# Kernel tuning notes

Measured on AMD Instinct MI355X. Metric: run time of the kernel, lower is better.

Reference implementation:

```python
import jax, jax.numpy as jnp
import numpy as np

# hypercfg constants (init_kwargs)
AUX = 0.05
L1W = 5.0
VPW = 1.0
VNW = 1.0


def _lsa_square(cost):
    """Jonker-Volgenant shortest-augmenting-path Hungarian on a square numpy
    cost matrix. Returns rows[j] = row assigned to column j. Runs on host,
    mirroring the original CPU scipy.optimize.linear_sum_assignment call."""
    n = cost.shape[0]
    INF = np.inf
    u = np.zeros(n + 1)
    v = np.zeros(n + 1)
    p = np.zeros(n + 1, dtype=np.int64)   # p[j] = row matched to column j (1-indexed)
    way = np.zeros(n + 1, dtype=np.int64)
    for i in range(1, n + 1):
        p[0] = i
        j0 = 0
        minv = np.full(n + 1, INF)
        used = np.zeros(n + 1, dtype=bool)
        while True:
            used[j0] = True
            i0 = p[j0]
            cur = cost[i0 - 1, :] - u[i0] - v[1:]
            free = ~used[1:]
            upd = free & (cur < minv[1:])
            minv1 = minv[1:]
            minv1[upd] = cur[upd]
            way1 = way[1:]
            way1[upd] = j0
            mfree = np.where(free, minv1, INF)
            j1 = int(np.argmin(mfree)) + 1
            delta = mfree[j1 - 1]
            used_idx = np.nonzero(used)[0]
            u[p[used_idx]] += delta
            v[used_idx] -= delta
            minv1[free] -= delta
            j0 = j1
            if p[j0] == 0:
                break
        while j0 != 0:
            j1 = way[j0]
            p[j0] = p[j1]
            j0 = j1
    return p[1:] - 1


def _match(cost_mk):
    """Rectangular assignment, cost [M, K] with K <= M: pad with a constant
    column block (dummy columns cost the same for any row, so the real K
    columns get the optimal assignment, matching scipy on rectangles)."""
    M, K = cost_mk.shape
    pad = np.zeros((M, M), dtype=np.float64)
    pad[:, :K] = cost_mk
    rows = _lsa_square(pad)
    return rows[:K]


def _cost(meta_points, meta_visibles, gtpoints, gtvisibles):
    # meta_points: [S,B,L,M,2]  gtpoints: [S,B,K,2]
    # meta_visibles: [S,B,M,1]  gtvisibles: [S,B,K,1]
    S, B, L, M, _ = meta_points.shape
    # pairwise L1 cost: [S,B,L,M,K]
    diff = jnp.abs(meta_points[:, :, :, :, None, :] - gtpoints[:, :, None, None, :, :]).sum(-1)
    # delta[l] = L - (l+1), per-layer slack (torch.linspace(1, L, L))
    delta = (L - jnp.arange(1, L + 1, dtype=meta_points.dtype)) * AUX
    cost_p_ml = jax.nn.relu(diff - delta[None, None, :, None, None])
    gtv = gtvisibles[:, :, :, 0][:, :, None, :]          # [S,B,1,K]
    cost_p = gtv * cost_p_ml.mean(2)                     # [S,B,M,K]
    cost_vp = -gtv * jnp.log(meta_visibles)              # [S,B,M,1] -> [S,B,M,K]
    cost_vn = -(1.0 - gtv) * jnp.log(1.0 - meta_visibles)
    cost = L1W * cost_p + VPW * cost_vp + VNW * cost_vn  # [S,B,M,K]
    return cost.mean(0)                                  # mean over shots -> [B,M,K]


def setup_inputs() -> dict:
    key = jax.random.key(0)
    ks = jax.random.split(key, 5)
    S, B, L, M, K = 6, 16, 8, 256, 128
    meta_points = jax.random.uniform(ks[0], (S, B, L, M, 2), dtype=jnp.float32)
    # keep probabilities strictly inside (0,1) so log() is finite
    meta_visibles = jax.random.uniform(ks[1], (S, B, M, 1), dtype=jnp.float32) * 0.9 + 0.05
    covisibles = jax.random.uniform(ks[2], (B, K), dtype=jnp.float32)
    gtpoints = jax.random.uniform(ks[3], (S, B, K, 2), dtype=jnp.float32)
    gtvisibles = (jax.random.uniform(ks[4], (S, B, K, 1)) > 0.5).astype(jnp.float32)
    return {
        "meta_points": meta_points,
        "meta_visibles": meta_visibles,
        "covisibles": covisibles,
        "gtpoints": gtpoints,
        "gtvisibles": gtvisibles,
    }


def reference(meta_points, meta_visibles, covisibles, gtpoints, gtvisibles):
    # covisibles only provides the batch size in the original module
    cost = np.asarray(jax.jit(_cost)(meta_points, meta_visibles, gtpoints, gtvisibles))
    bs = cost.shape[0]
    # per-batch Hungarian on host (sequential data-dependent algorithm);
    # result[b, k] = meta index matched to keypoint k (already kp-sorted,
    # matching the argsort-reorder in the torch code)
    out = np.stack([_match(cost[b]) for b in range(bs)])
    return jnp.asarray(out, dtype=jnp.int64)
```

## Files before the change

### kernel.cpp

```cpp
#include <hip/hip_runtime.h>
#include <math.h>


#define S_ 6
#define B_ 16
#define L_ 8
#define M_ 256
#define K_ 128

__global__ void cost_kernel(const float* __restrict__ mp,
                            const float* __restrict__ mv,
                            const float* __restrict__ gt,
                            const float* __restrict__ gv,
                            float* __restrict__ cost)
{
#pragma clang fp contract(off)
    const int b = blockIdx.x;
    const int m = blockIdx.y;
    const int k = threadIdx.x;

    float accS = 0.0f;
    for (int s = 0; s < S_; ++s) {
        const int sb = s * B_ + b;
        const float gx = gt[(sb * K_ + k) * 2 + 0];
        const float gy = gt[(sb * K_ + k) * 2 + 1];
        float accL = 0.0f;
#pragma unroll
        for (int l = 0; l < L_; ++l) {
            const int base = ((sb * L_ + l) * M_ + m) * 2;
            const float dx = fabsf(mp[base + 0] - gx);
            const float dy = fabsf(mp[base + 1] - gy);
            const float diff = dx + dy;
            const float dl = (float)(L_ - (l + 1)) * 0.05f;
            const float t = diff - dl;
            accL += fmaxf(t, 0.0f);
        }
        const float meanL = accL * 0.125f;
        const float mvv = mv[sb * M_ + m];
        const float gtv = gv[sb * K_ + k];
        const float lp = -logf(mvv);
        const float ln = -logf(1.0f - mvv);
        const float val = (gtv != 0.0f) ? (5.0f * meanL + lp) : ln;
        accS += val;
    }
    cost[(b * M_ + m) * K_ + k] = accS * (1.0f / 6.0f);
}

__device__ __forceinline__ double bits2d(int lo, int hi) {
    const unsigned long long u =
        ((unsigned long long)(unsigned)hi << 32) | (unsigned)lo;
    return __longlong_as_double((long long)u);
}
__device__ __forceinline__ void d2bits(double d, int& lo, int& hi) {
    const unsigned long long u = (unsigned long long)__double_as_longlong(d);
    lo = (int)(u & 0xffffffffull);
    hi = (int)(u >> 32);
}

__global__ __launch_bounds__(64, 1) void match_kernel(const float* __restrict__ cost,
                                                      int* __restrict__ out)
{
#pragma clang fp contract(off)
    const int b = blockIdx.x;
    const int lane = threadIdx.x;
    const float* C = cost + (size_t)b * M_ * K_;
    const double INF = __builtin_inf();
    const int BIG = 0x7fffffff;

    __shared__ float  C_lds[M_ * K_];
    __shared__ double u_lds[257];
    __shared__ int    p_lds[257];

    for (int t = lane; t < (M_ * K_) / 4; t += 64)
        ((float4*)C_lds)[t] = ((const float4*)C)[t];

    for (int t = lane; t < 257; t += 64) {
        u_lds[t] = 0.0;
        p_lds[t] = (t >= 129) ? (t - 128) : 0;
    }
    __syncthreads();

    double v0 = 0.0, v1 = 0.0, v2 = 0.0, v3 = 0.0;

    for (int i = 129; i <= 256; ++i) {
        int used = 0;
        const int pj0 = p_lds[2 * lane + 1];
        const int pj1 = p_lds[2 * lane + 2];
        const int pj2 = p_lds[2 * lane + 129];
        const int pj3 = p_lds[2 * lane + 130];
        double ur0 = u_lds[pj0], ur1 = u_lds[pj1];
        double ur2 = u_lds[pj2], ur3 = u_lds[pj3];
        const double up0 = ur0, up1 = ur1, up2 = ur2, up3 = ur3;

        float2 cc = *(const float2*)(C_lds + (i - 1) * K_ + 2 * lane);
        double u_i0 = 0.0;
        int j1 = 0;
        double usum = 0.0;

        for (;;) {
            double cd0 = ((double)cc.x - u_i0) - v0;
            double cd1 = ((double)cc.y - u_i0) - v1;
            double cd2 = (0.0 - u_i0) - v2;
            double cd3 = (0.0 - u_i0) - v3;
            if (used & 1) cd0 = INF;
            if (used & 2) cd1 = INF;
            if (used & 4) cd2 = INF;
            if (used & 8) cd3 = INF;

            const double m01 = fmin(cd0, cd1);
            const double m23 = fmin(cd2, cd3);
            double bv = fmin(m01, m23);

            int lo, hi; d2bits(bv, lo, hi);
#define MIN_STAGE(CTRL, RM)                                                      \
            {                                                                    \
                const int nlo = __builtin_amdgcn_update_dpp(lo, lo, CTRL, RM, 0xf, false); \
                const int nhi = __builtin_amdgcn_update_dpp(hi, hi, CTRL, RM, 0xf, false); \
                const double mv2 = fmin(bits2d(lo, hi), bits2d(nlo, nhi));       \
                d2bits(mv2, lo, hi);                                             \
            }
            MIN_STAGE(0x111, 0xf)
            MIN_STAGE(0x112, 0xf)
            MIN_STAGE(0x114, 0xf)
            MIN_STAGE(0x118, 0xf)
            MIN_STAGE(0x142, 0xa)
            MIN_STAGE(0x143, 0xc)
#undef MIN_STAGE
            const int mlo = __builtin_amdgcn_readlane(lo, 63);
            const int mhi = __builtin_amdgcn_readlane(hi, 63);
            const double delta = bits2d(mlo, mhi);

            int jr = BIG;
            if (cd1 == delta) jr = 2 * lane + 2;
            if (cd0 == delta) jr = 2 * lane + 1;
            int jd = BIG;
            if (cd3 == delta) jd = 2 * lane + 130;
            if (cd2 == delta) jd = 2 * lane + 129;
            const unsigned long long br = __ballot(jr != BIG);
            const unsigned long long bd = __ballot(jd != BIG);
            const unsigned long long bb = br ? br : bd;
            const int cand = (br != 0ull) ? jr : jd;
            j1 = __builtin_amdgcn_readlane(cand, (int)__builtin_ctzll(bb));

            int ol, sl;
            if (j1 >= 129) { ol = (j1 - 129) >> 1; sl = 2 + ((j1 - 129) & 1); }
            else           { ol = (j1 - 1) >> 1;   sl = (j1 - 1) & 1; }
            const int psel = (sl == 0) ? pj0 : (sl == 1) ? pj1 : (sl == 2) ? pj2 : pj3;
            const int i0n = (j1 >= 129) ? (j1 - 128)
                                        : __builtin_amdgcn_readlane(psel, ol);

            const int rown = (i0n > 0 ? i0n : 1) - 1;
            const float2 ccn = *(const float2*)(C_lds + rown * K_ + 2 * lane);

            usum += delta;
            if (used & 1) { ur0 += delta; v0 -= delta; }
            if (used & 2) { ur1 += delta; v1 -= delta; }
            if (used & 4) { ur2 += delta; v2 -= delta; }
            if (used & 8) { ur3 += delta; v3 -= delta; }

            const double usel = (sl == 0) ? up0 : (sl == 1) ? up1 : (sl == 2) ? up2 : up3;
            int ulo, uhi; d2bits(usel, ulo, uhi);
            const double u_n = bits2d(__builtin_amdgcn_readlane(ulo, ol),
                                      __builtin_amdgcn_readlane(uhi, ol));

            if (i0n == 0) break;

            if (lane == ol) used |= (1 << sl);
            u_i0 = u_n;
            cc = ccn;
        }

        __syncthreads();
        if (used & 1) u_lds[pj0] = ur0;
        if (used & 2) u_lds[pj1] = ur1;
        if (used & 4) u_lds[pj2] = ur2;
        if (used & 8) u_lds[pj3] = ur3;
        if (lane == 0) { p_lds[j1] = i; u_lds[i] = usum; }
        __syncthreads();
    }

    for (int j = lane; j < K_; j += 64)
        out[b * K_ + j] = p_lds[j + 1] - 1;
}

extern "C" void kernel_launch(void* const* d_in, const int* in_sizes, int n_in,
                              void* d_out, int out_size, void* d_ws, size_t ws_size,
                              hipStream_t stream) {
    const float* mp = (const float*)d_in[0];
    const float* mv = (const float*)d_in[1];
    const float* gt = (const float*)d_in[3];
    const float* gv = (const float*)d_in[4];
    int* out = (int*)d_out;
    float* cost = (float*)d_ws;

    dim3 gridA(B_, M_);
    cost_kernel<<<gridA, K_, 0, stream>>>(mp, mv, gt, gv, cost);
    match_kernel<<<B_, 64, 0, stream>>>(cost, out);
}
```

Before: 1.419 ms.

## Exploit constant dummy-column costs to skip per-step dummy min reduction

Dummy columns all have zero cost, so their reduced cost depends only on v. The per-step wavefront minimum therefore covers only the real columns. The best remaining dummy column is tracked through a separate max-v selection, with the next two candidates and their cost rows prefetched. This removes half of the per-step comparisons and the second ballot, but adds a DPP argmax reduction whenever a dummy column is chosen, and it changes how ties are broken.

```diff
diff --git a/kernel.cpp b/kernel.cpp
--- a/kernel.cpp
+++ b/kernel.cpp
@@ -57,6 +57,36 @@
     hi = (int)(u >> 32);
 }
 
+__device__ __forceinline__ void dummy_sel(double v2, double v3, bool e2, bool e3,
+                                          int lane, int& jd, double& vs) {
+    const double NINF = -__builtin_inf();
+    double bv = e2 ? v2 : NINF;
+    int bj = e2 ? (2 * lane + 129) : 0x7fffffff;
+    if (e3 && (v3 > bv)) { bv = v3; bj = 2 * lane + 130; }
+    int lo, hi; d2bits(bv, lo, hi);
+    int idx = bj;
+#define SEL_STAGE(CTRL, RM)                                                      \
+    {                                                                            \
+        const int nlo = __builtin_amdgcn_update_dpp(lo, lo, CTRL, RM, 0xf, false);   \
+        const int nhi = __builtin_amdgcn_update_dpp(hi, hi, CTRL, RM, 0xf, false);   \
+        const int nix = __builtin_amdgcn_update_dpp(idx, idx, CTRL, RM, 0xf, false); \
+        const double nv = bits2d(nlo, nhi);                                      \
+        const double cv = bits2d(lo, hi);                                        \
+        const bool take = (nv > cv) || (nv == cv && nix < idx);                  \
+        lo = take ? nlo : lo; hi = take ? nhi : hi; idx = take ? nix : idx;      \
+    }
+    SEL_STAGE(0x111, 0xf)
+    SEL_STAGE(0x112, 0xf)
+    SEL_STAGE(0x114, 0xf)
+    SEL_STAGE(0x118, 0xf)
+    SEL_STAGE(0x142, 0xa)
+    SEL_STAGE(0x143, 0xc)
+#undef SEL_STAGE
+    jd = __builtin_amdgcn_readlane(idx, 63);
+    vs = bits2d(__builtin_amdgcn_readlane(lo, 63),
+                __builtin_amdgcn_readlane(hi, 63));
+}
+
 __global__ __launch_bounds__(64, 1) void match_kernel(const float* __restrict__ cost,
                                                       int* __restrict__ out)
 {
@@ -86,13 +116,22 @@
         int used = 0;
         const int pj0 = p_lds[2 * lane + 1];
         const int pj1 = p_lds[2 * lane + 2];
-        const int pj2 = p_lds[2 * lane + 129];
-        const int pj3 = p_lds[2 * lane + 130];
         double ur0 = u_lds[pj0], ur1 = u_lds[pj1];
-        double ur2 = u_lds[pj2], ur3 = u_lds[pj3];
+        double ur2 = u_lds[2 * lane + 1];
+        double ur3 = u_lds[2 * lane + 2];
         const double up0 = ur0, up1 = ur1, up2 = ur2, up3 = ur3;
 
-        float2 cc = *(const float2*)(C_lds + (i - 1) * K_ + 2 * lane);
+        int jdA, jdB; double vAs, vBs;
+        dummy_sel(v2, v3, true, true, lane, jdA, vAs);
+        {
+            const bool e2 = (jdA != 2 * lane + 129);
+            const bool e3 = (jdA != 2 * lane + 130);
+            dummy_sel(v2, v3, e2, e3, lane, jdB, vBs);
+        }
+        float2 cc  = *(const float2*)(C_lds + (i - 1) * K_ + 2 * lane);
+        float2 ccA = *(const float2*)(C_lds + ((jdA == BIG ? 129 : jdA) - 129) * K_ + 2 * lane);
+        float2 ccB = *(const float2*)(C_lds + ((jdB == BIG ? 129 : jdB) - 129) * K_ + 2 * lane);
+
         double u_i0 = 0.0;
         int j1 = 0;
         double usum = 0.0;
@@ -100,16 +139,9 @@
         for (;;) {
             double cd0 = ((double)cc.x - u_i0) - v0;
             double cd1 = ((double)cc.y - u_i0) - v1;
-            double cd2 = (0.0 - u_i0) - v2;
-            double cd3 = (0.0 - u_i0) - v3;
             if (used & 1) cd0 = INF;
             if (used & 2) cd1 = INF;
-            if (used & 4) cd2 = INF;
-            if (used & 8) cd3 = INF;
-
-            const double m01 = fmin(cd0, cd1);
-            const double m23 = fmin(cd2, cd3);
-            double bv = fmin(m01, m23);
+            double bv = fmin(cd0, cd1);
 
             int lo, hi; d2bits(bv, lo, hi);
 #define MIN_STAGE(CTRL, RM)                                                      \
@@ -126,31 +158,13 @@
             MIN_STAGE(0x142, 0xa)
             MIN_STAGE(0x143, 0xc)
 #undef MIN_STAGE
-            const int mlo = __builtin_amdgcn_readlane(lo, 63);
-            const int mhi = __builtin_amdgcn_readlane(hi, 63);
-            const double delta = bits2d(mlo, mhi);
-
-            int jr = BIG;
-            if (cd1 == delta) jr = 2 * lane + 2;
-            if (cd0 == delta) jr = 2 * lane + 1;
-            int jd = BIG;
-            if (cd3 == delta) jd = 2 * lane + 130;
-            if (cd2 == delta) jd = 2 * lane + 129;
-            const unsigned long long br = __ballot(jr != BIG);
-            const unsigned long long bd = __ballot(jd != BIG);
-            const unsigned long long bb = br ? br : bd;
-            const int cand = (br != 0ull) ? jr : jd;
-            j1 = __builtin_amdgcn_readlane(cand, (int)__builtin_ctzll(bb));
-
-            int ol, sl;
-            if (j1 >= 129) { ol = (j1 - 129) >> 1; sl = 2 + ((j1 - 129) & 1); }
-            else           { ol = (j1 - 1) >> 1;   sl = (j1 - 1) & 1; }
-            const int psel = (sl == 0) ? pj0 : (sl == 1) ? pj1 : (sl == 2) ? pj2 : pj3;
-            const int i0n = (j1 >= 129) ? (j1 - 128)
-                                        : __builtin_amdgcn_readlane(psel, ol);
-
-            const int rown = (i0n > 0 ? i0n : 1) - 1;
-            const float2 ccn = *(const float2*)(C_lds + rown * K_ + 2 * lane);
+            const double Rmin = bits2d(__builtin_amdgcn_readlane(lo, 63),
+                                       __builtin_amdgcn_readlane(hi, 63));
+
+            const double Dmin = (0.0 - u_i0) - vAs;
+
+            const double delta = fmin(Rmin, Dmin);
+            const bool realw = (Rmin <= Dmin);
 
             usum += delta;
             if (used & 1) { ur0 += delta; v0 -= delta; }
@@ -158,23 +172,43 @@
             if (used & 4) { ur2 += delta; v2 -= delta; }
             if (used & 8) { ur3 += delta; v3 -= delta; }
 
-            const double usel = (sl == 0) ? up0 : (sl == 1) ? up1 : (sl == 2) ? up2 : up3;
-            int ulo, uhi; d2bits(usel, ulo, uhi);
-            const double u_n = bits2d(__builtin_amdgcn_readlane(ulo, ol),
-                                      __builtin_amdgcn_readlane(uhi, ol));
-
-            if (i0n == 0) break;
-
-            if (lane == ol) used |= (1 << sl);
-            u_i0 = u_n;
-            cc = ccn;
+            if (realw) {
+                int jr = BIG;
+                if (cd1 == delta) jr = 2 * lane + 2;
+                if (cd0 == delta) jr = 2 * lane + 1;
+                const unsigned long long bb = __ballot(jr != BIG);
+                j1 = __builtin_amdgcn_readlane(jr, (int)__builtin_ctzll(bb));
+                const int ol = (j1 - 1) >> 1, sl = (j1 - 1) & 1;
+                const int psel = sl ? pj1 : pj0;
+                const int i0n = __builtin_amdgcn_readlane(psel, ol);
+                if (i0n == 0) break;
+                const double usel = sl ? up1 : up0;
+                int ulo, uhi; d2bits(usel, ulo, uhi);
+                u_i0 = bits2d(__builtin_amdgcn_readlane(ulo, ol),
+                              __builtin_amdgcn_readlane(uhi, ol));
+                if (lane == ol) used |= (1 << sl);
+                cc = *(const float2*)(C_lds + (i0n - 1) * K_ + 2 * lane);
+            } else {
+                j1 = jdA;
+                const int ol = (jdA - 129) >> 1, sl = 2 + ((jdA - 129) & 1);
+                const double usel = (sl == 2) ? up2 : up3;
+                int ulo, uhi; d2bits(usel, ulo, uhi);
+                u_i0 = bits2d(__builtin_amdgcn_readlane(ulo, ol),
+                              __builtin_amdgcn_readlane(uhi, ol));
+                if (lane == ol) used |= (1 << sl);
+                cc = ccA; ccA = ccB; jdA = jdB; vAs = vBs;
+                const bool e2 = !(used & 4) && (jdA != 2 * lane + 129);
+                const bool e3 = !(used & 8) && (jdA != 2 * lane + 130);
+                dummy_sel(v2, v3, e2, e3, lane, jdB, vBs);
+                ccB = *(const float2*)(C_lds + ((jdB == BIG ? 129 : jdB) - 129) * K_ + 2 * lane);
+            }
         }
 
         __syncthreads();
         if (used & 1) u_lds[pj0] = ur0;
         if (used & 2) u_lds[pj1] = ur1;
-        if (used & 4) u_lds[pj2] = ur2;
-        if (used & 8) u_lds[pj3] = ur3;
+        if (used & 4) u_lds[2 * lane + 1] = ur2;
+        if (used & 8) u_lds[2 * lane + 2] = ur3;
         if (lane == 0) { p_lds[j1] = i; u_lds[i] = usum; }
         __syncthreads();
     }
```

After: 1.949 ms. 37.4% more time.

## Replace dummy-column scan with sorted prefetch queue in Hungarian augment loop

Applied to the files above, without the earlier changes.

Dummy columns all have zero cost, so their reduced cost within a row is just -u_i0 - v. The order in which they become minimal is therefore set by the largest v among unused dummies. The inner loop now does its wave-wide min reduction only over the real columns. Dummy candidates come from a small queue of up to four entries, refilled through a max-reduction over the dummy v values together with their u and cost rows. This removes half the per-step comparison and reduction work but adds refill reductions, branching and many more live registers.

```diff
diff --git a/kernel.cpp b/kernel.cpp
--- a/kernel.cpp
+++ b/kernel.cpp
@@ -57,6 +57,35 @@
     hi = (int)(u >> 32);
 }
 
+#define MIN_STAGE(lo, hi, CTRL, RM)                                              \
+{                                                                                \
+    const int nlo = __builtin_amdgcn_update_dpp(lo, lo, CTRL, RM, 0xf, false);   \
+    const int nhi = __builtin_amdgcn_update_dpp(hi, hi, CTRL, RM, 0xf, false);   \
+    const double m2 = fmin(bits2d(lo, hi), bits2d(nlo, nhi));                    \
+    d2bits(m2, lo, hi);                                                          \
+}
+#define MAX_STAGE(lo, hi, CTRL, RM)                                              \
+{                                                                                \
+    const int nlo = __builtin_amdgcn_update_dpp(lo, lo, CTRL, RM, 0xf, false);   \
+    const int nhi = __builtin_amdgcn_update_dpp(hi, hi, CTRL, RM, 0xf, false);   \
+    const double m2 = fmax(bits2d(lo, hi), bits2d(nlo, nhi));                    \
+    d2bits(m2, lo, hi);                                                          \
+}
+#define LADDER_MIN(lo, hi)          \
+    MIN_STAGE(lo, hi, 0x111, 0xf)   \
+    MIN_STAGE(lo, hi, 0x112, 0xf)   \
+    MIN_STAGE(lo, hi, 0x114, 0xf)   \
+    MIN_STAGE(lo, hi, 0x118, 0xf)   \
+    MIN_STAGE(lo, hi, 0x142, 0xa)   \
+    MIN_STAGE(lo, hi, 0x143, 0xc)
+#define LADDER_MAX(lo, hi)          \
+    MAX_STAGE(lo, hi, 0x111, 0xf)   \
+    MAX_STAGE(lo, hi, 0x112, 0xf)   \
+    MAX_STAGE(lo, hi, 0x114, 0xf)   \
+    MAX_STAGE(lo, hi, 0x118, 0xf)   \
+    MAX_STAGE(lo, hi, 0x142, 0xa)   \
+    MAX_STAGE(lo, hi, 0x143, 0xc)
+
 __global__ __launch_bounds__(64, 1) void match_kernel(const float* __restrict__ cost,
                                                       int* __restrict__ out)
 {
@@ -65,6 +94,7 @@
     const int lane = threadIdx.x;
     const float* C = cost + (size_t)b * M_ * K_;
     const double INF = __builtin_inf();
+    const double NINF = -__builtin_inf();
     const int BIG = 0x7fffffff;
 
     __shared__ float  C_lds[M_ * K_];
@@ -84,13 +114,48 @@
 
     for (int i = 129; i <= 256; ++i) {
         int used = 0;
+        int dq = 0;
         const int pj0 = p_lds[2 * lane + 1];
         const int pj1 = p_lds[2 * lane + 2];
-        const int pj2 = p_lds[2 * lane + 129];
-        const int pj3 = p_lds[2 * lane + 130];
         double ur0 = u_lds[pj0], ur1 = u_lds[pj1];
-        double ur2 = u_lds[pj2], ur3 = u_lds[pj3];
-        const double up0 = ur0, up1 = ur1, up2 = ur2, up3 = ur3;
+        double ur2 = u_lds[2 * lane + 1];
+        double ur3 = u_lds[2 * lane + 2];
+        const double up0 = ur0, up1 = ur1;
+
+        double kv0 = 0, kv1 = 0, kv2q = 0, kv3q = 0;
+        int    kj0 = 0, kj1 = 0, kj2q = 0, kj3q = 0;
+        double ku0 = 0, ku1 = 0, ku2q = 0, ku3q = 0;
+        float  kcx0 = 0, kcx1 = 0, kcx2 = 0, kcx3 = 0;
+        float  kcy0 = 0, kcy1 = 0, kcy2 = 0, kcy3 = 0;
+        int head = 0, tail = 0;
+
+        auto refill = [&]() {
+            const bool e2 = !(dq & 1), e3 = !(dq & 2);
+            double bb = e2 ? v2 : NINF;
+            if (e3 && (v3 > bb)) bb = v3;
+            int lo, hi; d2bits(bb, lo, hi);
+            LADDER_MAX(lo, hi)
+            const double rv = bits2d(__builtin_amdgcn_readlane(lo, 63),
+                                     __builtin_amdgcn_readlane(hi, 63));
+            if (rv == NINF) return;
+            int cand = BIG;
+            if (e3 && (v3 == rv)) cand = 2 * lane + 130;
+            if (e2 && (v2 == rv)) cand = 2 * lane + 129;
+            const unsigned long long bl = __ballot(cand != BIG);
+            const int rj = __builtin_amdgcn_readlane(cand, (int)__builtin_ctzll(bl));
+            const int olr = (rj - 129) >> 1, slr = (rj - 129) & 1;
+            if (lane == olr) dq |= (1 << slr);
+            const double kun = u_lds[rj - 128];
+            const float2 kcc = *(const float2*)(C_lds + (rj - 129) * K_ + 2 * lane);
+            const int ts = tail & 3;
+            if (ts == 0) { kv0 = rv; kj0 = rj; ku0 = kun; kcx0 = kcc.x; kcy0 = kcc.y; }
+            else if (ts == 1) { kv1 = rv; kj1 = rj; ku1 = kun; kcx1 = kcc.x; kcy1 = kcc.y; }
+            else if (ts == 2) { kv2q = rv; kj2q = rj; ku2q = kun; kcx2 = kcc.x; kcy2 = kcc.y; }
+            else { kv3q = rv; kj3q = rj; ku3q = kun; kcx3 = kcc.x; kcy3 = kcc.y; }
+            tail++;
+        };
+        refill();
+        refill();
 
         float2 cc = *(const float2*)(C_lds + (i - 1) * K_ + 2 * lane);
         double u_i0 = 0.0;
@@ -100,81 +165,72 @@
         for (;;) {
             double cd0 = ((double)cc.x - u_i0) - v0;
             double cd1 = ((double)cc.y - u_i0) - v1;
-            double cd2 = (0.0 - u_i0) - v2;
-            double cd3 = (0.0 - u_i0) - v3;
             if (used & 1) cd0 = INF;
             if (used & 2) cd1 = INF;
-            if (used & 4) cd2 = INF;
-            if (used & 8) cd3 = INF;
-
-            const double m01 = fmin(cd0, cd1);
-            const double m23 = fmin(cd2, cd3);
-            double bv = fmin(m01, m23);
-
+            double bv = fmin(cd0, cd1);
             int lo, hi; d2bits(bv, lo, hi);
-#define MIN_STAGE(CTRL, RM)                                                      \
-            {                                                                    \
-                const int nlo = __builtin_amdgcn_update_dpp(lo, lo, CTRL, RM, 0xf, false); \
-                const int nhi = __builtin_amdgcn_update_dpp(hi, hi, CTRL, RM, 0xf, false); \
-                const double mv2 = fmin(bits2d(lo, hi), bits2d(nlo, nhi));       \
-                d2bits(mv2, lo, hi);                                             \
+            LADDER_MIN(lo, hi)
+            const double Rmin = bits2d(__builtin_amdgcn_readlane(lo, 63),
+                                       __builtin_amdgcn_readlane(hi, 63));
+
+            const int qn = tail - head;
+            const int hs = head & 3;
+            const double kvh = (hs == 0) ? kv0 : (hs == 1) ? kv1 : (hs == 2) ? kv2q : kv3q;
+            const double Dmin = (qn > 0) ? ((0.0 - u_i0) - kvh) : INF;
+
+            const double delta = fmin(Rmin, Dmin);
+            const bool realw = (Rmin <= Dmin);
+
+            if (realw) {
+                int jr = BIG;
+                if (cd1 == delta) jr = 2 * lane + 2;
+                if (cd0 == delta) jr = 2 * lane + 1;
+                const unsigned long long bb2 = __ballot(jr != BIG);
+                j1 = __builtin_amdgcn_readlane(jr, (int)__builtin_ctzll(bb2));
+                const int ol = (j1 - 1) >> 1, sl = (j1 - 1) & 1;
+                const int psel = sl ? pj1 : pj0;
+                const int i0n = __builtin_amdgcn_readlane(psel, ol);
+                const int rown = (i0n > 0 ? i0n : 1) - 1;
+                const float2 ccn = *(const float2*)(C_lds + rown * K_ + 2 * lane);
+                usum += delta;
+                if (used & 1) { ur0 += delta; v0 -= delta; }
+                if (used & 2) { ur1 += delta; v1 -= delta; }
+                if (used & 4) { ur2 += delta; v2 -= delta; }
+                if (used & 8) { ur3 += delta; v3 -= delta; }
+                const double usel = sl ? up1 : up0;
+                int ulo, uhi; d2bits(usel, ulo, uhi);
+                const double u_n = bits2d(__builtin_amdgcn_readlane(ulo, ol),
+                                          __builtin_amdgcn_readlane(uhi, ol));
+                if (i0n == 0) break;
+                if (lane == ol) used |= (1 << sl);
+                u_i0 = u_n;
+                cc = ccn;
+            } else {
+                const int kjh = (hs == 0) ? kj0 : (hs == 1) ? kj1 : (hs == 2) ? kj2q : kj3q;
+                const double kuh = (hs == 0) ? ku0 : (hs == 1) ? ku1 : (hs == 2) ? ku2q : ku3q;
+                const float ccx = (hs == 0) ? kcx0 : (hs == 1) ? kcx1 : (hs == 2) ? kcx2 : kcx3;
+                const float ccy = (hs == 0) ? kcy0 : (hs == 1) ? kcy1 : (hs == 2) ? kcy2 : kcy3;
+                j1 = kjh;
+                head++;
+                usum += delta;
+                if (used & 1) { ur0 += delta; v0 -= delta; }
+                if (used & 2) { ur1 += delta; v1 -= delta; }
+                if (used & 4) { ur2 += delta; v2 -= delta; }
+                if (used & 8) { ur3 += delta; v3 -= delta; }
+                const int ol = (j1 - 129) >> 1, sl = 2 + ((j1 - 129) & 1);
+                if (lane == ol) used |= (1 << sl);
+                u_i0 = kuh;
+                cc.x = ccx; cc.y = ccy;
             }
-            MIN_STAGE(0x111, 0xf)
-            MIN_STAGE(0x112, 0xf)
-            MIN_STAGE(0x114, 0xf)
-            MIN_STAGE(0x118, 0xf)
-            MIN_STAGE(0x142, 0xa)
-            MIN_STAGE(0x143, 0xc)
-#undef MIN_STAGE
-            const int mlo = __builtin_amdgcn_readlane(lo, 63);
-            const int mhi = __builtin_amdgcn_readlane(hi, 63);
-            const double delta = bits2d(mlo, mhi);
-
-            int jr = BIG;
-            if (cd1 == delta) jr = 2 * lane + 2;
-            if (cd0 == delta) jr = 2 * lane + 1;
-            int jd = BIG;
-            if (cd3 == delta) jd = 2 * lane + 130;
-            if (cd2 == delta) jd = 2 * lane + 129;
-            const unsigned long long br = __ballot(jr != BIG);
-            const unsigned long long bd = __ballot(jd != BIG);
-            const unsigned long long bb = br ? br : bd;
-            const int cand = (br != 0ull) ? jr : jd;
-            j1 = __builtin_amdgcn_readlane(cand, (int)__builtin_ctzll(bb));
-
-            int ol, sl;
-            if (j1 >= 129) { ol = (j1 - 129) >> 1; sl = 2 + ((j1 - 129) & 1); }
-            else           { ol = (j1 - 1) >> 1;   sl = (j1 - 1) & 1; }
-            const int psel = (sl == 0) ? pj0 : (sl == 1) ? pj1 : (sl == 2) ? pj2 : pj3;
-            const int i0n = (j1 >= 129) ? (j1 - 128)
-                                        : __builtin_amdgcn_readlane(psel, ol);
-
-            const int rown = (i0n > 0 ? i0n : 1) - 1;
-            const float2 ccn = *(const float2*)(C_lds + rown * K_ + 2 * lane);
-
-            usum += delta;
-            if (used & 1) { ur0 += delta; v0 -= delta; }
-            if (used & 2) { ur1 += delta; v1 -= delta; }
-            if (used & 4) { ur2 += delta; v2 -= delta; }
-            if (used & 8) { ur3 += delta; v3 -= delta; }
-
-            const double usel = (sl == 0) ? up0 : (sl == 1) ? up1 : (sl == 2) ? up2 : up3;
-            int ulo, uhi; d2bits(usel, ulo, uhi);
-            const double u_n = bits2d(__builtin_amdgcn_readlane(ulo, ol),
-                                      __builtin_amdgcn_readlane(uhi, ol));
-
-            if (i0n == 0) break;
-
-            if (lane == ol) used |= (1 << sl);
-            u_i0 = u_n;
-            cc = ccn;
+
+            if (tail - head < 4) refill();
         }
 
         __syncthreads();
         if (used & 1) u_lds[pj0] = ur0;
         if (used & 2) u_lds[pj1] = ur1;
-        if (used & 4) u_lds[pj2] = ur2;
-        if (used & 8) u_lds[pj3] = ur3;
+        if (used & 4) u_lds[2 * lane + 1] = ur2;
+        if (used & 8) u_lds[2 * lane + 2] = ur3;
         if (lane == 0) { p_lds[j1] = i; u_lds[i] = usum; }
         __syncthreads();
     }
```

Result: slower. 3.509 ms (+147.3%).
